# Kernel optimization log

Hardware: AMD Instinct MI355X
Metric: run time of the kernel (lower is better)

The kernel has to match this reference:

```python
import jax, jax.numpy as jnp
import numpy as np

B, N, T, NOUT = 32, 2048, 500, 2
NE = 1638                      # excitatory cells; Ni = N - NE
MUE = 0.5                      # constant external drive
PR = 0.1                       # pr_plastic
DT_TAUSINV = 0.1               # dt / taus_long
WREC_INIT = 1.0 * 10.0 / np.sqrt(N * PR)   # scale_plastic * taum / sqrt(N*pr)


def setup_inputs() -> dict:
    key = jax.random.key(0)
    k1, k2, k3, k4, k5 = jax.random.split(key, 5)
    u0 = jax.random.normal(k1, (B, N), jnp.float32)
    ext = 0.1 * jax.random.normal(k2, (T, B, N), jnp.float32)  # stim+feedback+noise
    mask = (jax.random.uniform(k3, (N, N)) < PR).astype(jnp.float32)
    weight_rec = mask * WREC_INIT * jax.random.uniform(k4, (N, N), jnp.float32)
    weight_sign = jnp.concatenate([jnp.ones(NE, jnp.float32), -jnp.ones(N - NE, jnp.float32)])
    weight_out = 0.1 * jax.random.normal(k5, (N, NOUT), jnp.float32)
    dt_tausinv = jnp.full((1, N), DT_TAUSINV, jnp.float32)
    return dict(u0=u0, ext=ext, weight_rec=weight_rec, mask=mask,
                weight_sign=weight_sign, weight_out=weight_out, dt_tausinv=dt_tausinv)


def reference(u0, ext, weight_rec, mask, weight_sign, weight_out, dt_tausinv):
    # weight_dale(): mask * relu(w_rec) * sign(pre-synaptic cell), applied per column
    w_dale_t = (mask * jax.nn.relu(weight_rec) * weight_sign[None, :]).T  # [N_pre, N_post]

    def step(u, ext_t):
        r = jax.nn.sigmoid(3.0 * u - 2.0)                     # activation(u)
        drive = r @ w_dale_t + MUE + ext_t                    # recurrent + external input
        u_new = u * (1.0 - dt_tausinv) + drive * dt_tausinv   # leaky integration
        out = r @ weight_out                                  # weight_out_mixed readout
        return u_new, (u_new, out)

    _, (usave, outsave) = jax.lax.scan(step, u0, ext)
    return usave, outsave  # [T,B,N], [T,B,Nout]
```

## Files before the change

### kernel.cpp

```cpp
#include <hip/hip_runtime.h>

#define NTOT   2048
#define BATCH  32
#define TSTEPS 500
#define NBLK   256
#define COLS   8
#define CAP    320
#define RELEMS (BATCH * NTOT)
#define OUT_BASE (TSTEPS * RELEMS)
#define NGRP   8
#define GRPSZ  32
#define GLOBI  128

static __device__ __forceinline__ float act(float u) {
  return 1.0f / (1.0f + expf(2.0f - 3.0f * u));
}

static __device__ __forceinline__ void st_coh(float* p, float v) {
  __hip_atomic_store(p, v, __ATOMIC_RELAXED, __HIP_MEMORY_SCOPE_AGENT);
}
static __device__ __forceinline__ float ld_coh(const float* p) {
  return __hip_atomic_load(p, __ATOMIC_RELAXED, __HIP_MEMORY_SCOPE_AGENT);
}

__global__ void alif_init(unsigned int* bar) { bar[threadIdx.x] = 0u; }

template <bool FRESH>
__global__ __launch_bounds__(1024, 4) void alif_main(
    const float* __restrict__ u0,
    const float* __restrict__ ext,
    const float* __restrict__ wrec,
    const float* __restrict__ mask,
    const float* __restrict__ sign,
    const float* __restrict__ dtv,
    float* __restrict__ rbuf,
    float* __restrict__ usave,
    unsigned int* __restrict__ bar) {
  const int tid  = threadIdx.x;
  const int lane = tid & 63;
  const int wv   = tid >> 6;
  const int nw   = blockDim.x >> 6;
  const int KR   = NTOT / nw;

  __shared__ uint2 csr[COLS * CAP];
  __shared__ float red[32][32];
  __shared__ int   wcnt[16];
  __shared__ int   nnzs[COLS];
  __shared__ int   Lcol[COLS];

  for (int clb = 0; clb < COLS; ++clb) {
    const int c = blockIdx.x * COLS + clb;
    const float* __restrict__ mrow = mask + c * NTOT;
    int cnt = 0;
    for (int k0 = wv * KR; k0 < wv * KR + KR; k0 += 64)
      cnt += __popcll(__ballot(mrow[k0 + lane] != 0.0f));
    if (lane == 0) wcnt[wv] = cnt;
    __syncthreads();
    int base = 0, total = 0;
    for (int w2 = 0; w2 < nw; ++w2) {
      if (w2 < wv) base += wcnt[w2];
      total += wcnt[w2];
    }
    for (int k0 = wv * KR; k0 < wv * KR + KR; k0 += 64) {
      const int k = k0 + lane;
      const float mv = mrow[k];
      const bool nz = (mv != 0.0f);
      const unsigned long long bal = __ballot(nz);
      if (nz) {
        const int pos = base + __popcll(bal & ((1ull << lane) - 1ull));
        const float w = mv * fmaxf(wrec[c * NTOT + k], 0.0f) * sign[k];
        if (pos < CAP) csr[clb * CAP + pos] = make_uint2(__float_as_uint(w), (unsigned)(k * BATCH));
      }
      base += __popcll(bal);
    }
    if (tid == 0) {
      const int nn = (total < CAP) ? total : CAP;
      nnzs[clb] = nn;
      Lcol[clb] = (nn + 31) & ~31;
    }
    __syncthreads();
  }
  for (int clb = 0; clb < COLS; ++clb)
    for (int i = nnzs[clb] + tid; i < Lcol[clb]; i += blockDim.x)
      csr[clb * CAP + i] = make_uint2(0u, 0u);

  const int grp = tid >> 5;
  const int b   = tid & 31;
  const int cl  = grp & 7;
  const int s   = grp >> 3;
  const int S   = blockDim.x >> 8;
  const int lS  = 31 - __clz((unsigned)S);
  const int c   = blockIdx.x * COLS + cl;
  const bool own = (s == 0);

  float u = 0.f, dtc = 0.f, omd = 0.f;
  if (own) {
    dtc = dtv[c];
    omd = 1.0f - dtc;
    u = u0[b * NTOT + c];
    st_coh(&rbuf[c * BATCH + b], act(u));
  }
  const int g = blockIdx.x & (NGRP - 1);

  for (int t = 0; t < TSTEPS; ++t) {
    __syncthreads();
    if (tid == 0) {
      const unsigned prev =
          __hip_atomic_fetch_add(&bar[16 * g], 1u, __ATOMIC_RELAXED, __HIP_MEMORY_SCOPE_AGENT);
      if (((prev + 1u) & (GRPSZ - 1u)) == 0u)
        __hip_atomic_fetch_add(&bar[GLOBI], 1u, __ATOMIC_RELAXED, __HIP_MEMORY_SCOPE_AGENT);
      const unsigned gt = (unsigned)(t + 1) * NGRP;
      while (__hip_atomic_load(&bar[GLOBI], __ATOMIC_RELAXED, __HIP_MEMORY_SCOPE_AGENT) < gt)
        __builtin_amdgcn_s_sleep(1);
    }
    __syncthreads();

    const float e = own ? ext[t * RELEMS + b * NTOT + c] : 0.0f;

    const int Lc = Lcol[cl] >> lS;
    const uint2* __restrict__ ce = csr + cl * CAP + s * Lc;
    const size_t rph = FRESH ? (size_t)t : (size_t)(t & 1);
    const float* __restrict__ rrow = rbuf + rph * RELEMS + b;
    float a0 = 0.f, a1 = 0.f, a2 = 0.f, a3 = 0.f;
    float a4 = 0.f, a5 = 0.f, a6 = 0.f, a7 = 0.f;
    for (int i = 0; i < Lc; i += 8) {
      const uint2 e0 = ce[i],     e1 = ce[i + 1], e2 = ce[i + 2], e3 = ce[i + 3];
      const uint2 e4 = ce[i + 4], e5 = ce[i + 5], e6 = ce[i + 6], e7 = ce[i + 7];
      if (FRESH) {
        a0 = fmaf(rrow[e0.y], __uint_as_float(e0.x), a0);
        a1 = fmaf(rrow[e1.y], __uint_as_float(e1.x), a1);
        a2 = fmaf(rrow[e2.y], __uint_as_float(e2.x), a2);
        a3 = fmaf(rrow[e3.y], __uint_as_float(e3.x), a3);
        a4 = fmaf(rrow[e4.y], __uint_as_float(e4.x), a4);
        a5 = fmaf(rrow[e5.y], __uint_as_float(e5.x), a5);
        a6 = fmaf(rrow[e6.y], __uint_as_float(e6.x), a6);
        a7 = fmaf(rrow[e7.y], __uint_as_float(e7.x), a7);
      } else {
        a0 = fmaf(ld_coh(rrow + e0.y), __uint_as_float(e0.x), a0);
        a1 = fmaf(ld_coh(rrow + e1.y), __uint_as_float(e1.x), a1);
        a2 = fmaf(ld_coh(rrow + e2.y), __uint_as_float(e2.x), a2);
        a3 = fmaf(ld_coh(rrow + e3.y), __uint_as_float(e3.x), a3);
        a4 = fmaf(ld_coh(rrow + e4.y), __uint_as_float(e4.x), a4);
        a5 = fmaf(ld_coh(rrow + e5.y), __uint_as_float(e5.x), a5);
        a6 = fmaf(ld_coh(rrow + e6.y), __uint_as_float(e6.x), a6);
        a7 = fmaf(ld_coh(rrow + e7.y), __uint_as_float(e7.x), a7);
      }
    }
    red[grp][b] = (((a0 + a1) + (a2 + a3)) + ((a4 + a5) + (a6 + a7)));
    __syncthreads();

    if (own) {
      float rec = 0.f;
      for (int j = 0; j < S; ++j) rec += red[cl + 8 * j][b];
      const float drv = (rec + 0.5f) + e;
      u = u * omd + drv * dtc;
      const size_t wph = FRESH ? (size_t)(t + 1) : (size_t)((t + 1) & 1);
      st_coh(&rbuf[wph * RELEMS + c * BATCH + b], act(u));
      usave[t * RELEMS + b * NTOT + c] = u;
    }
  }
}

__global__ __launch_bounds__(256) void alif_readout(
    const float* __restrict__ u0,
    const float* __restrict__ usave,
    const float* __restrict__ wout,
    float* __restrict__ outs) {
  const int wg = blockIdx.x * 4 + (threadIdx.x >> 6);
  const int lane = threadIdx.x & 63;
  const int t = wg >> 5, b = wg & 31;
  float a0 = 0.f, a1 = 0.f;
  for (int k0 = 0; k0 < NTOT; k0 += 64) {
    const int k = k0 + lane;
    const float uv = (t == 0) ? u0[b * NTOT + k] : usave[(t - 1) * RELEMS + b * NTOT + k];
    const float r = act(uv);
    const float2 w2 = *(const float2*)(wout + k * 2);
    a0 = fmaf(r, w2.x, a0);
    a1 = fmaf(r, w2.y, a1);
  }
#pragma unroll
  for (int off = 32; off; off >>= 1) {
    a0 += __shfl_xor(a0, off, 64);
    a1 += __shfl_xor(a1, off, 64);
  }
  if (lane == 0) {
    outs[t * (BATCH * 2) + b * 2 + 0] = a0;
    outs[t * (BATCH * 2) + b * 2 + 1] = a1;
  }
}

extern "C" void kernel_launch(void* const* d_in, const int* in_sizes, int n_in,
                              void* d_out, int out_size, void* d_ws, size_t ws_size,
                              hipStream_t stream) {
  const float* u0   = (const float*)d_in[0];
  const float* ext  = (const float*)d_in[1];
  const float* wrec = (const float*)d_in[2];
  const float* mask = (const float*)d_in[3];
  const float* sign = (const float*)d_in[4];
  const float* wout = (const float*)d_in[5];
  const float* dtv  = (const float*)d_in[6];
  float* out = (float*)d_out;

  char* w = (char*)d_ws;
  unsigned int* bar  = (unsigned int*)w;
  float*        rbuf = (float*)(w + 1024);

  const size_t need = 1024 + (size_t)(TSTEPS + 1) * RELEMS * sizeof(float);
  const bool fresh = (ws_size >= need);

  alif_init<<<dim3(1), dim3(256), 0, stream>>>(bar);

  void* args[] = {(void*)&u0, (void*)&ext, (void*)&wrec, (void*)&mask, (void*)&sign,
                  (void*)&dtv, (void*)&rbuf, (void*)&out, (void*)&bar};

  const void* fn = fresh ? (const void*)alif_main<true> : (const void*)alif_main<false>;
  hipError_t err = hipLaunchCooperativeKernel(fn, dim3(NBLK), dim3(1024), args, 0, stream);
  if (err != hipSuccess) {
    (void)hipLaunchCooperativeKernel(fn, dim3(NBLK), dim3(256), args, 0, stream);
  }

  alif_readout<<<dim3(TSTEPS * BATCH / 4), dim3(256), 0, stream>>>(
      u0, out, wout, out + OUT_BASE);
}
```

Before: 2.988 ms.

## Give each thread four batch elements with float4 gathers and split nonzeros across more groups

Each thread now handles four consecutive batch entries of a column. In the fresh path it gathers them with one float4 load per nonzero instead of one scalar load. The nonzeros of each column are split over more slices (S equals the wave count, so 16 with 1024 threads), and padding is now a multiple of 4*S. The usave store for a step is deferred to after the next barrier, and the ext load is moved there too, so that work sits off the critical path between the barrier and the state update. This is meant to cut per-nonzero load instructions and shorten the serial chain per thread, at the cost of more padding, a larger reduction and strided 4-way scalar stores.

```diff
diff --git a/kernel.cpp b/kernel.cpp
--- a/kernel.cpp
+++ b/kernel.cpp
@@ -15,7 +15,6 @@
 static __device__ __forceinline__ float act(float u) {
   return 1.0f / (1.0f + expf(2.0f - 3.0f * u));
 }
-
 static __device__ __forceinline__ void st_coh(float* p, float v) {
   __hip_atomic_store(p, v, __ATOMIC_RELAXED, __HIP_MEMORY_SCOPE_AGENT);
 }
@@ -41,12 +40,13 @@
   const int wv   = tid >> 6;
   const int nw   = blockDim.x >> 6;
   const int KR   = NTOT / nw;
-
-  __shared__ uint2 csr[COLS * CAP];
-  __shared__ float red[32][32];
-  __shared__ int   wcnt[16];
-  __shared__ int   nnzs[COLS];
-  __shared__ int   Lcol[COLS];
+  const int S    = nw;
+
+  __shared__ uint2  csr[COLS * CAP];
+  __shared__ float4 red4[128][8];
+  __shared__ int    wcnt[16];
+  __shared__ int    nnzs[COLS];
+  __shared__ int    Lcol[COLS];
 
   for (int clb = 0; clb < COLS; ++clb) {
     const int c = blockIdx.x * COLS + clb;
@@ -76,7 +76,8 @@
     if (tid == 0) {
       const int nn = (total < CAP) ? total : CAP;
       nnzs[clb] = nn;
-      Lcol[clb] = (nn + 31) & ~31;
+      const int padm = 4 * S;
+      Lcol[clb] = (nn + padm - 1) & ~(padm - 1);
     }
     __syncthreads();
   }
@@ -84,21 +85,28 @@
     for (int i = nnzs[clb] + tid; i < Lcol[clb]; i += blockDim.x)
       csr[clb * CAP + i] = make_uint2(0u, 0u);
 
-  const int grp = tid >> 5;
-  const int b   = tid & 31;
+  const int grp = tid >> 3;
+  const int l8  = tid & 7;
+  const int b0  = l8 * 4;
   const int cl  = grp & 7;
   const int s   = grp >> 3;
-  const int S   = blockDim.x >> 8;
-  const int lS  = 31 - __clz((unsigned)S);
   const int c   = blockIdx.x * COLS + cl;
   const bool own = (s == 0);
 
-  float u = 0.f, dtc = 0.f, omd = 0.f;
+  float4 u4 = {0.f, 0.f, 0.f, 0.f}, uprev = u4;
+  float dtc = 0.f, omd = 0.f;
   if (own) {
     dtc = dtv[c];
     omd = 1.0f - dtc;
-    u = u0[b * NTOT + c];
-    st_coh(&rbuf[c * BATCH + b], act(u));
+    u4.x = u0[(b0 + 0) * NTOT + c];
+    u4.y = u0[(b0 + 1) * NTOT + c];
+    u4.z = u0[(b0 + 2) * NTOT + c];
+    u4.w = u0[(b0 + 3) * NTOT + c];
+    float* r0p = rbuf + c * BATCH + b0;
+    st_coh(r0p + 0, act(u4.x));
+    st_coh(r0p + 1, act(u4.y));
+    st_coh(r0p + 2, act(u4.z));
+    st_coh(r0p + 3, act(u4.w));
   }
   const int g = blockIdx.x & (NGRP - 1);
 
@@ -115,49 +123,96 @@
     }
     __syncthreads();
 
-    const float e = own ? ext[t * RELEMS + b * NTOT + c] : 0.0f;
-
-    const int Lc = Lcol[cl] >> lS;
+    float4 ev = {0.f, 0.f, 0.f, 0.f};
+    if (own) {
+      if (t > 0) {
+        float* up = usave + (size_t)(t - 1) * RELEMS + c;
+        up[(b0 + 0) * NTOT] = uprev.x;
+        up[(b0 + 1) * NTOT] = uprev.y;
+        up[(b0 + 2) * NTOT] = uprev.z;
+        up[(b0 + 3) * NTOT] = uprev.w;
+      }
+      const float* ep = ext + (size_t)t * RELEMS + c;
+      ev.x = ep[(b0 + 0) * NTOT];
+      ev.y = ep[(b0 + 1) * NTOT];
+      ev.z = ep[(b0 + 2) * NTOT];
+      ev.w = ep[(b0 + 3) * NTOT];
+    }
+
+    const int Lc = Lcol[cl] / S;
     const uint2* __restrict__ ce = csr + cl * CAP + s * Lc;
     const size_t rph = FRESH ? (size_t)t : (size_t)(t & 1);
-    const float* __restrict__ rrow = rbuf + rph * RELEMS + b;
-    float a0 = 0.f, a1 = 0.f, a2 = 0.f, a3 = 0.f;
-    float a4 = 0.f, a5 = 0.f, a6 = 0.f, a7 = 0.f;
-    for (int i = 0; i < Lc; i += 8) {
-      const uint2 e0 = ce[i],     e1 = ce[i + 1], e2 = ce[i + 2], e3 = ce[i + 3];
-      const uint2 e4 = ce[i + 4], e5 = ce[i + 5], e6 = ce[i + 6], e7 = ce[i + 7];
+    const float* __restrict__ rrow = rbuf + rph * RELEMS + b0;
+    float4 a0 = {0,0,0,0}, a1 = {0,0,0,0}, a2 = {0,0,0,0}, a3 = {0,0,0,0};
+    for (int i = 0; i < Lc; i += 4) {
+      const uint2 e0 = ce[i], e1 = ce[i + 1], e2 = ce[i + 2], e3 = ce[i + 3];
+      const float w0 = __uint_as_float(e0.x), w1 = __uint_as_float(e1.x);
+      const float w2 = __uint_as_float(e2.x), w3 = __uint_as_float(e3.x);
       if (FRESH) {
-        a0 = fmaf(rrow[e0.y], __uint_as_float(e0.x), a0);
-        a1 = fmaf(rrow[e1.y], __uint_as_float(e1.x), a1);
-        a2 = fmaf(rrow[e2.y], __uint_as_float(e2.x), a2);
-        a3 = fmaf(rrow[e3.y], __uint_as_float(e3.x), a3);
-        a4 = fmaf(rrow[e4.y], __uint_as_float(e4.x), a4);
-        a5 = fmaf(rrow[e5.y], __uint_as_float(e5.x), a5);
-        a6 = fmaf(rrow[e6.y], __uint_as_float(e6.x), a6);
-        a7 = fmaf(rrow[e7.y], __uint_as_float(e7.x), a7);
+        const float4 r0 = *reinterpret_cast<const float4*>(rrow + e0.y);
+        const float4 r1 = *reinterpret_cast<const float4*>(rrow + e1.y);
+        const float4 r2 = *reinterpret_cast<const float4*>(rrow + e2.y);
+        const float4 r3 = *reinterpret_cast<const float4*>(rrow + e3.y);
+        a0.x = fmaf(r0.x, w0, a0.x); a0.y = fmaf(r0.y, w0, a0.y);
+        a0.z = fmaf(r0.z, w0, a0.z); a0.w = fmaf(r0.w, w0, a0.w);
+        a1.x = fmaf(r1.x, w1, a1.x); a1.y = fmaf(r1.y, w1, a1.y);
+        a1.z = fmaf(r1.z, w1, a1.z); a1.w = fmaf(r1.w, w1, a1.w);
+        a2.x = fmaf(r2.x, w2, a2.x); a2.y = fmaf(r2.y, w2, a2.y);
+        a2.z = fmaf(r2.z, w2, a2.z); a2.w = fmaf(r2.w, w2, a2.w);
+        a3.x = fmaf(r3.x, w3, a3.x); a3.y = fmaf(r3.y, w3, a3.y);
+        a3.z = fmaf(r3.z, w3, a3.z); a3.w = fmaf(r3.w, w3, a3.w);
       } else {
-        a0 = fmaf(ld_coh(rrow + e0.y), __uint_as_float(e0.x), a0);
-        a1 = fmaf(ld_coh(rrow + e1.y), __uint_as_float(e1.x), a1);
-        a2 = fmaf(ld_coh(rrow + e2.y), __uint_as_float(e2.x), a2);
-        a3 = fmaf(ld_coh(rrow + e3.y), __uint_as_float(e3.x), a3);
-        a4 = fmaf(ld_coh(rrow + e4.y), __uint_as_float(e4.x), a4);
-        a5 = fmaf(ld_coh(rrow + e5.y), __uint_as_float(e5.x), a5);
-        a6 = fmaf(ld_coh(rrow + e6.y), __uint_as_float(e6.x), a6);
-        a7 = fmaf(ld_coh(rrow + e7.y), __uint_as_float(e7.x), a7);
-      }
-    }
-    red[grp][b] = (((a0 + a1) + (a2 + a3)) + ((a4 + a5) + (a6 + a7)));
+        a0.x = fmaf(ld_coh(rrow + e0.y + 0), w0, a0.x);
+        a0.y = fmaf(ld_coh(rrow + e0.y + 1), w0, a0.y);
+        a0.z = fmaf(ld_coh(rrow + e0.y + 2), w0, a0.z);
+        a0.w = fmaf(ld_coh(rrow + e0.y + 3), w0, a0.w);
+        a1.x = fmaf(ld_coh(rrow + e1.y + 0), w1, a1.x);
+        a1.y = fmaf(ld_coh(rrow + e1.y + 1), w1, a1.y);
+        a1.z = fmaf(ld_coh(rrow + e1.y + 2), w1, a1.z);
+        a1.w = fmaf(ld_coh(rrow + e1.y + 3), w1, a1.w);
+        a2.x = fmaf(ld_coh(rrow + e2.y + 0), w2, a2.x);
+        a2.y = fmaf(ld_coh(rrow + e2.y + 1), w2, a2.y);
+        a2.z = fmaf(ld_coh(rrow + e2.y + 2), w2, a2.z);
+        a2.w = fmaf(ld_coh(rrow + e2.y + 3), w2, a2.w);
+        a3.x = fmaf(ld_coh(rrow + e3.y + 0), w3, a3.x);
+        a3.y = fmaf(ld_coh(rrow + e3.y + 1), w3, a3.y);
+        a3.z = fmaf(ld_coh(rrow + e3.y + 2), w3, a3.z);
+        a3.w = fmaf(ld_coh(rrow + e3.y + 3), w3, a3.w);
+      }
+    }
+    float4 p;
+    p.x = (a0.x + a1.x) + (a2.x + a3.x);
+    p.y = (a0.y + a1.y) + (a2.y + a3.y);
+    p.z = (a0.z + a1.z) + (a2.z + a3.z);
+    p.w = (a0.w + a1.w) + (a2.w + a3.w);
+    red4[grp][l8] = p;
     __syncthreads();
 
     if (own) {
-      float rec = 0.f;
-      for (int j = 0; j < S; ++j) rec += red[cl + 8 * j][b];
-      const float drv = (rec + 0.5f) + e;
-      u = u * omd + drv * dtc;
+      float4 rec = {0.f, 0.f, 0.f, 0.f};
+      for (int j = 0; j < S; ++j) {
+        const float4 v = red4[8 * j + cl][l8];
+        rec.x += v.x; rec.y += v.y; rec.z += v.z; rec.w += v.w;
+      }
+      u4.x = u4.x * omd + ((rec.x + 0.5f) + ev.x) * dtc;
+      u4.y = u4.y * omd + ((rec.y + 0.5f) + ev.y) * dtc;
+      u4.z = u4.z * omd + ((rec.z + 0.5f) + ev.z) * dtc;
+      u4.w = u4.w * omd + ((rec.w + 0.5f) + ev.w) * dtc;
       const size_t wph = FRESH ? (size_t)(t + 1) : (size_t)((t + 1) & 1);
-      st_coh(&rbuf[wph * RELEMS + c * BATCH + b], act(u));
-      usave[t * RELEMS + b * NTOT + c] = u;
-    }
+      float* rp = rbuf + wph * RELEMS + c * BATCH + b0;
+      st_coh(rp + 0, act(u4.x));
+      st_coh(rp + 1, act(u4.y));
+      st_coh(rp + 2, act(u4.z));
+      st_coh(rp + 3, act(u4.w));
+      uprev = u4;
+    }
+  }
+  if (own) {
+    float* up = usave + (size_t)(TSTEPS - 1) * RELEMS + c;
+    up[(b0 + 0) * NTOT] = uprev.x;
+    up[(b0 + 1) * NTOT] = uprev.y;
+    up[(b0 + 2) * NTOT] = uprev.z;
+    up[(b0 + 3) * NTOT] = uprev.w;
   }
 }
 
```

Result: slower. 3.357 ms (+12.3%).

## Vectorize sparse gather to float4 per batch quad and split barrier release flags

Applied to the files above, without the earlier changes.

Each thread now handles four batch elements through a float4 gather per nonzero, instead of one batch element with scalar loads. The split is now 8 threads per column group and more k-splits, with reduction through a float4 shared array. This cuts load instruction count and CSR reads per FMA. The grid barrier also gains a last-arriver release that writes per-group flag words, so waiting blocks no longer all poll one global counter. The risks are fewer independent accumulators, so less memory-level parallelism per thread, and a changed non-FRESH path.

```diff
diff --git a/kernel.cpp b/kernel.cpp
--- a/kernel.cpp
+++ b/kernel.cpp
@@ -5,7 +5,8 @@
 #define TSTEPS 500
 #define NBLK   256
 #define COLS   8
-#define CAP    320
+#define NNZCAP 320
+#define CAP    322
 #define RELEMS (BATCH * NTOT)
 #define OUT_BASE (TSTEPS * RELEMS)
 #define NGRP   8
@@ -15,7 +16,6 @@
 static __device__ __forceinline__ float act(float u) {
   return 1.0f / (1.0f + expf(2.0f - 3.0f * u));
 }
-
 static __device__ __forceinline__ void st_coh(float* p, float v) {
   __hip_atomic_store(p, v, __ATOMIC_RELAXED, __HIP_MEMORY_SCOPE_AGENT);
 }
@@ -41,12 +41,14 @@
   const int wv   = tid >> 6;
   const int nw   = blockDim.x >> 6;
   const int KR   = NTOT / nw;
-
-  __shared__ uint2 csr[COLS * CAP];
-  __shared__ float red[32][32];
-  __shared__ int   wcnt[16];
-  __shared__ int   nnzs[COLS];
-  __shared__ int   Lcol[COLS];
+  const int S    = nw;
+  const int lS   = (nw == 16) ? 4 : 2;
+
+  __shared__ uint2  csr[COLS * CAP];
+  __shared__ float4 red4[128][8];
+  __shared__ int    wcnt[16];
+  __shared__ int    nnzs[COLS];
+  __shared__ int    Lcol[COLS];
 
   for (int clb = 0; clb < COLS; ++clb) {
     const int c = blockIdx.x * COLS + clb;
@@ -69,12 +71,13 @@
       if (nz) {
         const int pos = base + __popcll(bal & ((1ull << lane) - 1ull));
         const float w = mv * fmaxf(wrec[c * NTOT + k], 0.0f) * sign[k];
-        if (pos < CAP) csr[clb * CAP + pos] = make_uint2(__float_as_uint(w), (unsigned)(k * BATCH));
+        if (pos < NNZCAP)
+          csr[clb * CAP + pos] = make_uint2(__float_as_uint(w), (unsigned)(k * BATCH));
       }
       base += __popcll(bal);
     }
     if (tid == 0) {
-      const int nn = (total < CAP) ? total : CAP;
+      const int nn = (total < NNZCAP) ? total : NNZCAP;
       nnzs[clb] = nn;
       Lcol[clb] = (nn + 31) & ~31;
     }
@@ -84,14 +87,16 @@
     for (int i = nnzs[clb] + tid; i < Lcol[clb]; i += blockDim.x)
       csr[clb * CAP + i] = make_uint2(0u, 0u);
 
-  const int grp = tid >> 5;
-  const int b   = tid & 31;
-  const int cl  = grp & 7;
-  const int s   = grp >> 3;
-  const int S   = blockDim.x >> 8;
-  const int lS  = 31 - __clz((unsigned)S);
-  const int c   = blockIdx.x * COLS + cl;
-  const bool own = (s == 0);
+  const int grp8 = tid >> 3;
+  const int l8   = tid & 7;
+  const int b0g  = l8 * 4;
+  const int gcl  = grp8 & 7;
+  const int gs   = grp8 >> 3;
+
+  const bool own = (tid < 256);
+  const int  cl  = (tid >> 5) & 7;
+  const int  b   = tid & 31;
+  const int  c   = blockIdx.x * COLS + cl;
 
   float u = 0.f, dtc = 0.f, omd = 0.f;
   if (own) {
@@ -107,56 +112,64 @@
     if (tid == 0) {
       const unsigned prev =
           __hip_atomic_fetch_add(&bar[16 * g], 1u, __ATOMIC_RELAXED, __HIP_MEMORY_SCOPE_AGENT);
-      if (((prev + 1u) & (GRPSZ - 1u)) == 0u)
-        __hip_atomic_fetch_add(&bar[GLOBI], 1u, __ATOMIC_RELAXED, __HIP_MEMORY_SCOPE_AGENT);
-      const unsigned gt = (unsigned)(t + 1) * NGRP;
-      while (__hip_atomic_load(&bar[GLOBI], __ATOMIC_RELAXED, __HIP_MEMORY_SCOPE_AGENT) < gt)
+      if (((prev + 1u) & (GRPSZ - 1u)) == 0u) {
+        const unsigned pg =
+            __hip_atomic_fetch_add(&bar[GLOBI], 1u, __ATOMIC_RELAXED, __HIP_MEMORY_SCOPE_AGENT);
+        if (pg + 1u == (unsigned)(t + 1) * NGRP) {
+          for (int q = 0; q < NGRP; ++q)
+            __hip_atomic_store(&bar[16 * q + 8], (unsigned)(t + 1),
+                               __ATOMIC_RELAXED, __HIP_MEMORY_SCOPE_AGENT);
+        }
+      }
+      while (__hip_atomic_load(&bar[16 * g + 8], __ATOMIC_RELAXED, __HIP_MEMORY_SCOPE_AGENT)
+             < (unsigned)(t + 1))
         __builtin_amdgcn_s_sleep(1);
     }
     __syncthreads();
 
-    const float e = own ? ext[t * RELEMS + b * NTOT + c] : 0.0f;
-
-    const int Lc = Lcol[cl] >> lS;
-    const uint2* __restrict__ ce = csr + cl * CAP + s * Lc;
+    const float e = own ? ext[(size_t)t * RELEMS + b * NTOT + c] : 0.0f;
+
+    const int Lc = Lcol[gcl] >> lS;
+    const uint2* __restrict__ ce = csr + gcl * CAP + gs * Lc;
     const size_t rph = FRESH ? (size_t)t : (size_t)(t & 1);
-    const float* __restrict__ rrow = rbuf + rph * RELEMS + b;
-    float a0 = 0.f, a1 = 0.f, a2 = 0.f, a3 = 0.f;
-    float a4 = 0.f, a5 = 0.f, a6 = 0.f, a7 = 0.f;
-    for (int i = 0; i < Lc; i += 8) {
-      const uint2 e0 = ce[i],     e1 = ce[i + 1], e2 = ce[i + 2], e3 = ce[i + 3];
-      const uint2 e4 = ce[i + 4], e5 = ce[i + 5], e6 = ce[i + 6], e7 = ce[i + 7];
+    const float* __restrict__ rrow = rbuf + rph * RELEMS + b0g;
+    float4 a0 = {0,0,0,0}, a1 = {0,0,0,0};
+    for (int i = 0; i < Lc; i += 2) {
+      const uint2 e0 = ce[i], e1 = ce[i + 1];
+      const float w0 = __uint_as_float(e0.x), w1 = __uint_as_float(e1.x);
       if (FRESH) {
-        a0 = fmaf(rrow[e0.y], __uint_as_float(e0.x), a0);
-        a1 = fmaf(rrow[e1.y], __uint_as_float(e1.x), a1);
-        a2 = fmaf(rrow[e2.y], __uint_as_float(e2.x), a2);
-        a3 = fmaf(rrow[e3.y], __uint_as_float(e3.x), a3);
-        a4 = fmaf(rrow[e4.y], __uint_as_float(e4.x), a4);
-        a5 = fmaf(rrow[e5.y], __uint_as_float(e5.x), a5);
-        a6 = fmaf(rrow[e6.y], __uint_as_float(e6.x), a6);
-        a7 = fmaf(rrow[e7.y], __uint_as_float(e7.x), a7);
+        const float4 r0 = *reinterpret_cast<const float4*>(rrow + e0.y);
+        const float4 r1 = *reinterpret_cast<const float4*>(rrow + e1.y);
+        a0.x = fmaf(r0.x, w0, a0.x); a0.y = fmaf(r0.y, w0, a0.y);
+        a0.z = fmaf(r0.z, w0, a0.z); a0.w = fmaf(r0.w, w0, a0.w);
+        a1.x = fmaf(r1.x, w1, a1.x); a1.y = fmaf(r1.y, w1, a1.y);
+        a1.z = fmaf(r1.z, w1, a1.z); a1.w = fmaf(r1.w, w1, a1.w);
       } else {
-        a0 = fmaf(ld_coh(rrow + e0.y), __uint_as_float(e0.x), a0);
-        a1 = fmaf(ld_coh(rrow + e1.y), __uint_as_float(e1.x), a1);
-        a2 = fmaf(ld_coh(rrow + e2.y), __uint_as_float(e2.x), a2);
-        a3 = fmaf(ld_coh(rrow + e3.y), __uint_as_float(e3.x), a3);
-        a4 = fmaf(ld_coh(rrow + e4.y), __uint_as_float(e4.x), a4);
-        a5 = fmaf(ld_coh(rrow + e5.y), __uint_as_float(e5.x), a5);
-        a6 = fmaf(ld_coh(rrow + e6.y), __uint_as_float(e6.x), a6);
-        a7 = fmaf(ld_coh(rrow + e7.y), __uint_as_float(e7.x), a7);
-      }
-    }
-    red[grp][b] = (((a0 + a1) + (a2 + a3)) + ((a4 + a5) + (a6 + a7)));
+        a0.x = fmaf(ld_coh(rrow + e0.y + 0), w0, a0.x);
+        a0.y = fmaf(ld_coh(rrow + e0.y + 1), w0, a0.y);
+        a0.z = fmaf(ld_coh(rrow + e0.y + 2), w0, a0.z);
+        a0.w = fmaf(ld_coh(rrow + e0.y + 3), w0, a0.w);
+        a1.x = fmaf(ld_coh(rrow + e1.y + 0), w1, a1.x);
+        a1.y = fmaf(ld_coh(rrow + e1.y + 1), w1, a1.y);
+        a1.z = fmaf(ld_coh(rrow + e1.y + 2), w1, a1.z);
+        a1.w = fmaf(ld_coh(rrow + e1.y + 3), w1, a1.w);
+      }
+    }
+    float4 p;
+    p.x = a0.x + a1.x; p.y = a0.y + a1.y; p.z = a0.z + a1.z; p.w = a0.w + a1.w;
+    red4[grp8][l8] = p;
     __syncthreads();
 
     if (own) {
       float rec = 0.f;
-      for (int j = 0; j < S; ++j) rec += red[cl + 8 * j][b];
-      const float drv = (rec + 0.5f) + e;
-      u = u * omd + drv * dtc;
+      for (int j = 0; j < S; ++j) {
+        const float* pv = reinterpret_cast<const float*>(&red4[8 * j + cl][b >> 2]);
+        rec += pv[b & 3];
+      }
+      u = u * omd + ((rec + 0.5f) + e) * dtc;
       const size_t wph = FRESH ? (size_t)(t + 1) : (size_t)((t + 1) & 1);
       st_coh(&rbuf[wph * RELEMS + c * BATCH + b], act(u));
-      usave[t * RELEMS + b * NTOT + c] = u;
+      usave[(size_t)t * RELEMS + b * NTOT + c] = u;
     }
   }
 }
@@ -172,7 +185,7 @@
   float a0 = 0.f, a1 = 0.f;
   for (int k0 = 0; k0 < NTOT; k0 += 64) {
     const int k = k0 + lane;
-    const float uv = (t == 0) ? u0[b * NTOT + k] : usave[(t - 1) * RELEMS + b * NTOT + k];
+    const float uv = (t == 0) ? u0[b * NTOT + k] : usave[(size_t)(t - 1) * RELEMS + b * NTOT + k];
     const float r = act(uv);
     const float2 w2 = *(const float2*)(wout + k * 2);
     a0 = fmaf(r, w2.x, a0);
```

Measured after the change: 4.159 ms. 1.39x slower.

## Scale persistent grid to 512 blocks with 4 columns per block when occupancy allows

Applied to the files above, without the earlier changes.

Makes columns-per-block depend on grid size and launches 512 cooperative blocks of 1024 threads when occupancy reports at least two blocks per CU, so each block owns 4 columns and splits each column's sparse dot product across 8 sub-groups instead of 4. Per-column padding is replaced by one shared padded length equal to the block's maximum nnz. The barrier becomes two-level with 16 groups and the global counter moves to a new slot. The aim is shorter per-step gather chains and more resident parallelism, at the cost of more blocks in the per-step grid barrier and padding work on shorter columns. The 256-thread fallback launch is dropped.

```diff
diff --git a/kernel.cpp b/kernel.cpp
--- a/kernel.cpp
+++ b/kernel.cpp
@@ -3,19 +3,14 @@
 #define NTOT   2048
 #define BATCH  32
 #define TSTEPS 500
-#define NBLK   256
-#define COLS   8
 #define CAP    320
 #define RELEMS (BATCH * NTOT)
 #define OUT_BASE (TSTEPS * RELEMS)
-#define NGRP   8
-#define GRPSZ  32
-#define GLOBI  128
+#define GLOBI  255
 
 static __device__ __forceinline__ float act(float u) {
   return 1.0f / (1.0f + expf(2.0f - 3.0f * u));
 }
-
 static __device__ __forceinline__ void st_coh(float* p, float v) {
   __hip_atomic_store(p, v, __ATOMIC_RELAXED, __HIP_MEMORY_SCOPE_AGENT);
 }
@@ -41,15 +36,19 @@
   const int wv   = tid >> 6;
   const int nw   = blockDim.x >> 6;
   const int KR   = NTOT / nw;
-
-  __shared__ uint2 csr[COLS * CAP];
+  const int cpb  = NTOT / gridDim.x;
+  const int lcpb = (cpb == 8) ? 3 : 2;
+  const int S    = 32 >> lcpb;
+  const int lS   = 5 - lcpb;
+
+  __shared__ uint2 csr[8 * CAP];
   __shared__ float red[32][32];
   __shared__ int   wcnt[16];
-  __shared__ int   nnzs[COLS];
-  __shared__ int   Lcol[COLS];
-
-  for (int clb = 0; clb < COLS; ++clb) {
-    const int c = blockIdx.x * COLS + clb;
+  __shared__ int   nnzs[8];
+  __shared__ int   maxns;
+
+  for (int clb = 0; clb < cpb; ++clb) {
+    const int c = blockIdx.x * cpb + clb;
     const float* __restrict__ mrow = mask + c * NTOT;
     int cnt = 0;
     for (int k0 = wv * KR; k0 < wv * KR + KR; k0 += 64)
@@ -73,24 +72,26 @@
       }
       base += __popcll(bal);
     }
-    if (tid == 0) {
-      const int nn = (total < CAP) ? total : CAP;
-      nnzs[clb] = nn;
-      Lcol[clb] = (nn + 31) & ~31;
-    }
-    __syncthreads();
-  }
-  for (int clb = 0; clb < COLS; ++clb)
-    for (int i = nnzs[clb] + tid; i < Lcol[clb]; i += blockDim.x)
+    if (tid == 0) nnzs[clb] = (total < CAP) ? total : CAP;
+    __syncthreads();
+  }
+  if (tid == 0) {
+    int m = 0;
+    for (int i = 0; i < cpb; ++i) m = (nnzs[i] > m) ? nnzs[i] : m;
+    const int padm = 8 * S;
+    maxns = (m + padm - 1) & ~(padm - 1);
+  }
+  __syncthreads();
+  const int maxn = maxns;
+  for (int clb = 0; clb < cpb; ++clb)
+    for (int i = nnzs[clb] + tid; i < maxn; i += blockDim.x)
       csr[clb * CAP + i] = make_uint2(0u, 0u);
 
   const int grp = tid >> 5;
   const int b   = tid & 31;
-  const int cl  = grp & 7;
-  const int s   = grp >> 3;
-  const int S   = blockDim.x >> 8;
-  const int lS  = 31 - __clz((unsigned)S);
-  const int c   = blockIdx.x * COLS + cl;
+  const int cl  = grp & (cpb - 1);
+  const int s   = grp >> lcpb;
+  const int c   = blockIdx.x * cpb + cl;
   const bool own = (s == 0);
 
   float u = 0.f, dtc = 0.f, omd = 0.f;
@@ -100,24 +101,25 @@
     u = u0[b * NTOT + c];
     st_coh(&rbuf[c * BATCH + b], act(u));
   }
-  const int g = blockIdx.x & (NGRP - 1);
+  const unsigned ngrp = gridDim.x >> 5;
+  const int g = blockIdx.x & (ngrp - 1);
 
   for (int t = 0; t < TSTEPS; ++t) {
     __syncthreads();
     if (tid == 0) {
       const unsigned prev =
           __hip_atomic_fetch_add(&bar[16 * g], 1u, __ATOMIC_RELAXED, __HIP_MEMORY_SCOPE_AGENT);
-      if (((prev + 1u) & (GRPSZ - 1u)) == 0u)
+      if (((prev + 1u) & 31u) == 0u)
         __hip_atomic_fetch_add(&bar[GLOBI], 1u, __ATOMIC_RELAXED, __HIP_MEMORY_SCOPE_AGENT);
-      const unsigned gt = (unsigned)(t + 1) * NGRP;
+      const unsigned gt = (unsigned)(t + 1) * ngrp;
       while (__hip_atomic_load(&bar[GLOBI], __ATOMIC_RELAXED, __HIP_MEMORY_SCOPE_AGENT) < gt)
         __builtin_amdgcn_s_sleep(1);
     }
     __syncthreads();
 
-    const float e = own ? ext[t * RELEMS + b * NTOT + c] : 0.0f;
-
-    const int Lc = Lcol[cl] >> lS;
+    const float e = own ? ext[(size_t)t * RELEMS + b * NTOT + c] : 0.0f;
+
+    const int Lc = maxn >> lS;
     const uint2* __restrict__ ce = csr + cl * CAP + s * Lc;
     const size_t rph = FRESH ? (size_t)t : (size_t)(t & 1);
     const float* __restrict__ rrow = rbuf + rph * RELEMS + b;
@@ -151,12 +153,11 @@
 
     if (own) {
       float rec = 0.f;
-      for (int j = 0; j < S; ++j) rec += red[cl + 8 * j][b];
-      const float drv = (rec + 0.5f) + e;
-      u = u * omd + drv * dtc;
+      for (int j = 0; j < S; ++j) rec += red[j * cpb + cl][b];
+      u = u * omd + ((rec + 0.5f) + e) * dtc;
       const size_t wph = FRESH ? (size_t)(t + 1) : (size_t)((t + 1) & 1);
       st_coh(&rbuf[wph * RELEMS + c * BATCH + b], act(u));
-      usave[t * RELEMS + b * NTOT + c] = u;
+      usave[(size_t)t * RELEMS + b * NTOT + c] = u;
     }
   }
 }
@@ -172,7 +173,7 @@
   float a0 = 0.f, a1 = 0.f;
   for (int k0 = 0; k0 < NTOT; k0 += 64) {
     const int k = k0 + lane;
-    const float uv = (t == 0) ? u0[b * NTOT + k] : usave[(t - 1) * RELEMS + b * NTOT + k];
+    const float uv = (t == 0) ? u0[b * NTOT + k] : usave[(size_t)(t - 1) * RELEMS + b * NTOT + k];
     const float r = act(uv);
     const float2 w2 = *(const float2*)(wout + k * 2);
     a0 = fmaf(r, w2.x, a0);
@@ -214,9 +215,16 @@
                   (void*)&dtv, (void*)&rbuf, (void*)&out, (void*)&bar};
 
   const void* fn = fresh ? (const void*)alif_main<true> : (const void*)alif_main<false>;
-  hipError_t err = hipLaunchCooperativeKernel(fn, dim3(NBLK), dim3(1024), args, 0, stream);
-  if (err != hipSuccess) {
-    (void)hipLaunchCooperativeKernel(fn, dim3(NBLK), dim3(256), args, 0, stream);
+
+  int G = 256, nb = 0;
+  hipError_t oe = fresh
+      ? hipOccupancyMaxActiveBlocksPerMultiprocessor(&nb, alif_main<true>, 1024, 0)
+      : hipOccupancyMaxActiveBlocksPerMultiprocessor(&nb, alif_main<false>, 1024, 0);
+  if (oe == hipSuccess && nb >= 2) G = 512;
+
+  hipError_t err = hipLaunchCooperativeKernel(fn, dim3(G), dim3(1024), args, 0, stream);
+  if (err != hipSuccess && G == 512) {
+    (void)hipLaunchCooperativeKernel(fn, dim3(256), dim3(1024), args, 0, stream);
   }
 
   alif_readout<<<dim3(TSTEPS * BATCH / 4), dim3(256), 0, stream>>>(
```

Result: faster. 2.625 ms, median of 2 (-12.1%).
